# Optimization experiments

Measured on AMD Instinct MI355X. Metric: run time of the kernel, lower is better.

Reference implementation:

```python
import jax, jax.numpy as jnp
import numpy as np
import math

EPS = 1e-5
GROUPS = 32

def group_norm(x, gamma, beta, groups=GROUPS, eps=EPS):
    B, C, H, W = x.shape
    xr = x.reshape(B, groups, C // groups, H, W)
    m = xr.mean(axis=(2, 3, 4), keepdims=True)
    v = xr.var(axis=(2, 3, 4), keepdims=True)
    xr = (xr - m) * jax.lax.rsqrt(v + eps)
    x = xr.reshape(B, C, H, W)
    return x * gamma[None, :, None, None] + beta[None, :, None, None]

def swish(x):
    return x * jax.nn.sigmoid(x)

def conv2d(x, w, b=None, padding='SAME'):
    # x: NCHW, w: OIHW
    y = jax.lax.conv_general_dilated(x, w, window_strides=(1, 1), padding=padding,
                                     dimension_numbers=('NCHW', 'OIHW', 'NCHW'))
    if b is not None:
        y = y + b[None, :, None, None]
    return y

def setup_inputs() -> dict:
    key = jax.random.key(0)
    ks = jax.random.split(key, 24)
    B, C, H, W = 16, 256, 32, 32
    NE = 256  # noise_level_emb_dim
    s = 0.02
    inp = {
        'x': jax.random.normal(ks[0], (B, C, H, W), jnp.float32),
        'time_emb': jax.random.normal(ks[1], (B, NE), jnp.float32),
        'c': jax.random.normal(ks[2], (B, C, H, W), jnp.float32),
        # block1: GroupNorm + Swish + Conv3x3(dim -> dim_out)
        'gn1_g': jnp.ones((C,), jnp.float32),
        'gn1_b': jnp.zeros((C,), jnp.float32),
        'conv1_w': jax.random.normal(ks[3], (C, C, 3, 3), jnp.float32) * s,
        'conv1_b': jnp.zeros((C,), jnp.float32),
        # FeatureWiseAffine linear (use_affine_level=False): Linear(NE -> dim_out)
        'noise_w': jax.random.normal(ks[4], (C, NE), jnp.float32) * s,
        'noise_b': jnp.zeros((C,), jnp.float32),
        # block2: GroupNorm + Swish + Conv3x3(dim_out -> dim_out)
        'gn2_g': jnp.ones((C,), jnp.float32),
        'gn2_b': jnp.zeros((C,), jnp.float32),
        'conv2_w': jax.random.normal(ks[5], (C, C, 3, 3), jnp.float32) * s,
        'conv2_b': jnp.zeros((C,), jnp.float32),
        # c_func: Conv1x1(dim_out -> dim_out)
        'cfunc_w': jax.random.normal(ks[6], (C, C, 1, 1), jnp.float32) * s,
        'cfunc_b': jnp.zeros((C,), jnp.float32),
        # attention: GroupNorm, qkv Conv1x1 (no bias), out Conv1x1
        'attn_gn_g': jnp.ones((C,), jnp.float32),
        'attn_gn_b': jnp.zeros((C,), jnp.float32),
        'qkv_w': jax.random.normal(ks[7], (3 * C, C, 1, 1), jnp.float32) * s,
        'out_w': jax.random.normal(ks[8], (C, C, 1, 1), jnp.float32) * s,
        'out_b': jnp.zeros((C,), jnp.float32),
    }
    return inp

def reference(x, time_emb, c,
              gn1_g, gn1_b, conv1_w, conv1_b,
              noise_w, noise_b,
              gn2_g, gn2_b, conv2_w, conv2_b,
              cfunc_w, cfunc_b,
              attn_gn_g, attn_gn_b, qkv_w, out_w, out_b):
    B, C, H, W = x.shape
    # ---- ResnetBlock ----
    h = conv2d(swish(group_norm(x, gn1_g, gn1_b)), conv1_w, conv1_b)
    # FeatureWiseAffine (additive): h + Linear(time_emb) broadcast over HxW
    h = h + (time_emb @ noise_w.T + noise_b)[:, :, None, None]
    h = conv2d(swish(group_norm(h, gn2_g, gn2_b)), conv2_w, conv2_b)
    h = conv2d(c, cfunc_w, cfunc_b) + h
    h = h + x  # res_conv is Identity since dim == dim_out
    # ---- SelfAttention (n_head=1) ----
    n = group_norm(h, attn_gn_g, attn_gn_b)
    qkv = conv2d(n, qkv_w)                       # [B, 3C, H, W]
    q, k, v = jnp.split(qkv.reshape(B, 3 * C, H * W), 3, axis=1)  # each [B, C, HW]
    scores = jnp.einsum('bcs,bct->bst', q, k) / math.sqrt(C)      # [B, HW, HW]
    attn = jax.nn.softmax(scores, axis=-1)
    o = jnp.einsum('bst,bct->bcs', attn, v).reshape(B, C, H, W)
    o = conv2d(o, out_w, out_b)
    return o + h
```

## Files before the change

kernel.cpp:

```cpp
#include <hip/hip_runtime.h>
#include <hip/hip_bf16.h>
#include <math.h>

typedef __hip_bfloat16 bf16;
typedef short short8 __attribute__((ext_vector_type(8)));
typedef float floatx4 __attribute__((ext_vector_type(4)));

#define NB 16
#define NC 256
#define NHW 1024
#define NNE 256
#define NP (NB*NC*NHW)

__device__ __forceinline__ unsigned short f2bu(float f){
  bf16 h = (bf16)f; return *(unsigned short*)&h;
}

template<bool SWISH>
__global__ void gn_t_kernel(const float* __restrict__ src, const float* __restrict__ gamma,
                            const float* __restrict__ beta, short* __restrict__ xp){
  int b = blockIdx.x >> 5, g = blockIdx.x & 31;
  const int GSZ = 8*NHW;
  size_t base = ((size_t)b*NC + g*8)*NHW;
  int tid = threadIdx.x;
  float s = 0.f, ss = 0.f;
  for (int i = tid; i < GSZ; i += 256){
    float v = src[base+i];
    s += v; ss += v*v;
  }
  __shared__ float rs[256], rq[256];
  rs[tid] = s; rq[tid] = ss;
  __syncthreads();
  for (int off=128; off>0; off>>=1){
    if (tid < off){ rs[tid]+=rs[tid+off]; rq[tid]+=rq[tid+off]; }
    __syncthreads();
  }
  float mean = rs[0] * (1.f/GSZ);
  float var  = rq[0] * (1.f/GSZ) - mean*mean;
  float inv  = rsqrtf(var + 1e-5f);
  float gm[8], bt[8];
  #pragma unroll
  for (int j=0;j<8;j++){ gm[j] = gamma[g*8+j]*inv; bt[j] = beta[g*8+j]; }
  short* dst = xp + (((size_t)b*8 + (g>>2))*NHW)*32 + (g&3)*8;
  for (int px = tid; px < NHW; px += 256){
    short8 pk;
    #pragma unroll
    for (int j=0;j<8;j++){
      float v = (src[base + j*NHW + px] - mean)*gm[j] + bt[j];
      if (SWISH) v = v / (1.f + __expf(-v));
      pk[j] = (short)f2bu(v);
    }
    *(short8*)(dst + (size_t)px*32) = pk;
  }
}

template<bool SWISH>
__global__ void gn_post_kernel(const float* __restrict__ src, const float* __restrict__ st,
                               const float* __restrict__ gamma, const float* __restrict__ beta,
                               short* __restrict__ xp){
  int b = blockIdx.x >> 5, g = blockIdx.x & 31;
  size_t base = ((size_t)b*NC + g*8)*NHW;
  int tid = threadIdx.x;
  float s  = st[(b*32+g)*2+0];
  float ss = st[(b*32+g)*2+1];
  float mean = s * (1.f/8192.f);
  float var  = ss * (1.f/8192.f) - mean*mean;
  float inv  = rsqrtf(var + 1e-5f);
  float gm[8], bt[8];
  #pragma unroll
  for (int j=0;j<8;j++){ gm[j] = gamma[g*8+j]*inv; bt[j] = beta[g*8+j]; }
  short* dst = xp + (((size_t)b*8 + (g>>2))*NHW)*32 + (g&3)*8;
  for (int px = tid; px < NHW; px += 256){
    short8 pk;
    #pragma unroll
    for (int j=0;j<8;j++){
      float v = (src[base + j*NHW + px] - mean)*gm[j] + bt[j];
      if (SWISH) v = v / (1.f + __expf(-v));
      pk[j] = (short)f2bu(v);
    }
    *(short8*)(dst + (size_t)px*32) = pk;
  }
}

__global__ void wprep3_kernel(const float* __restrict__ w1, const float* __restrict__ w2,
                              short* __restrict__ wp1, short* __restrict__ wp2,
                              float* __restrict__ st){
  int co = blockIdx.x & 255;
  const float* w = (blockIdx.x < 256) ? w1 : w2;
  short* wp = (blockIdx.x < 256) ? wp1 : wp2;
  int tid = threadIdx.x;
  if (blockIdx.x == 0){
    for (int i=tid;i<2048;i+=256) st[i] = 0.f;
  }
  __shared__ float tmp[2304];
  for (int i=tid;i<2304;i+=256) tmp[i] = w[(size_t)co*2304 + i];
  __syncthreads();
  for (int j=tid;j<2304;j+=256){
    int tap = j>>8, ci = j&255;
    wp[(((size_t)tap*8 + (ci>>5))*NC + co)*32 + (ci&31)] = (short)f2bu(tmp[ci*9 + tap]);
  }
}

__global__ void wprep1_kernel(const float* __restrict__ wq, const float* __restrict__ wc,
                              const float* __restrict__ wo,
                              short* __restrict__ wqp, short* __restrict__ wcp,
                              short* __restrict__ wop){
  int blk = blockIdx.x, tid = threadIdx.x;
  if (blk < 768){
    float v = wq[(size_t)blk*256 + tid];
    wqp[(((size_t)(tid>>5))*768 + blk)*32 + (tid&31)] = (short)f2bu(v);
  } else if (blk < 1024){
    int co = blk - 768;
    float v = wc[(size_t)co*256 + tid];
    wcp[(((size_t)(tid>>5))*256 + co)*32 + (tid&31)] = (short)f2bu(v);
  } else {
    int co = blk - 1024;
    float v = wo[(size_t)co*256 + tid];
    wop[(((size_t)(tid>>5))*256 + co)*32 + (tid&31)] = (short)f2bu(v);
  }
}

__global__ void cvtc_kernel(const float* __restrict__ c_in, short* __restrict__ cp){
  int pxc = blockIdx.x, cc = blockIdx.y, b = blockIdx.z, tid = threadIdx.x;
  __shared__ float ld[32][257];
  size_t gbase = ((size_t)b*NC + cc*32)*NHW + pxc*256;
  for (int j=0;j<32;j++) ld[j][tid] = c_in[gbase + (size_t)j*NHW + tid];
  __syncthreads();
  short* dst = cp + (((size_t)b*8 + cc)*NHW + pxc*256)*32;
  for (int it=0;it<4;it++){
    int pxl = it*64 + (tid>>2), ckl = tid&3;
    short8 pk;
    #pragma unroll
    for (int e=0;e<8;e++) pk[e] = (short)f2bu(ld[ckl*8+e][pxl]);
    *(short8*)(dst + (size_t)pxl*32 + ckl*8) = pk;
  }
}

__global__ void noise_kernel(const float* __restrict__ emb, const float* __restrict__ w,
                             const float* __restrict__ bias, float* __restrict__ na){
  int b = blockIdx.x, c = threadIdx.x;
  __shared__ float e[NNE];
  e[c] = emb[b*NNE + c];
  __syncthreads();
  float acc = bias[c];
  for (int k=0;k<NNE;k++) acc += e[k]*w[c*NNE+k];
  na[b*NC + c] = acc;
}

#define XSTR 264
__global__ __launch_bounds__(256,2)
void conv3_mfma_kernel(const short* __restrict__ xp, const short* __restrict__ wp,
                       const float* __restrict__ bias, const float* __restrict__ bias_bc,
                       const float* __restrict__ addf, float* __restrict__ out,
                       float* __restrict__ st){
  const int b = blockIdx.y, y0 = blockIdx.x;
  const int tid = threadIdx.x, wave = tid>>6, lane = tid&63;
  const int quad = lane>>4, lm = lane&15;
  __shared__ short Xs[3*34*XSTR];

  if (tid < 192){
    int r = tid>>6, side = (tid>>5)&1, ck = tid&31;
    short8 z = {0,0,0,0,0,0,0,0};
    *(short8*)&Xs[((r*34) + side*33)*XSTR + ck*8] = z;
  }
  for (int it=0; it<12; ++it){
    int idx = it*256 + tid;
    int r = idx>>10, rem = idx&1023;
    int x = rem>>5, ch = rem&31;
    int y = y0 - 1 + r;
    short8 v = {0,0,0,0,0,0,0,0};
    if ((unsigned)y < 32u)
      v = *(const short8*)(xp + (((size_t)b*8 + (ch>>2))*NHW + y*32 + x)*32 + (ch&3)*8);
    *(short8*)&Xs[(r*34 + x + 1)*XSTR + ch*8] = v;
  }
  __syncthreads();

  floatx4 acc[4][2];
  #pragma unroll
  for (int mt=0;mt<4;mt++)
    #pragma unroll
    for (int nt=0;nt<2;nt++) acc[mt][nt] = (floatx4){0.f,0.f,0.f,0.f};

  const int co_w = wave*64;
  const int aoff = (co_w + lm)*32 + quad*8;

  auto ldA = [&](int j, short8 a[4]){
    const short* p = wp + (size_t)j*NC*32 + aoff;
    #pragma unroll
    for (int mt=0;mt<4;mt++) a[mt] = *(const short8*)(p + mt*(16*32));
  };
  auto ldB = [&](int j, short8 bf[2]){
    int tap = j>>3, kk = j&7;
    int dy = (tap*11)>>5;
    int dxp = tap - dy*3;
    int base = (lm+dxp)*XSTR + quad*8 + kk*32 + dy*(34*XSTR);
    #pragma unroll
    for (int nt=0;nt<2;nt++)
      bf[nt] = *(const short8*)&Xs[base + nt*(16*XSTR)];
  };

  short8 A[4][4], Bf[4][2];
  ldA(0,A[0]); ldB(0,Bf[0]);
  ldA(1,A[1]); ldB(1,Bf[1]);
  ldA(2,A[2]); ldB(2,Bf[2]);
  ldA(3,A[3]); ldB(3,Bf[3]);
  for (int it=0; it<72; it+=4){
    #pragma unroll
    for (int u=0;u<4;u++){
      #pragma unroll
      for (int mt=0;mt<4;mt++)
        #pragma unroll
        for (int nt=0;nt<2;nt++)
          acc[mt][nt] = __builtin_amdgcn_mfma_f32_16x16x32_bf16(A[u][mt], Bf[u][nt], acc[mt][nt], 0,0,0);
      int j = it + 4 + u; if (j > 71) j = 71;
      ldA(j, A[u]); ldB(j, Bf[u]);
    }
  }

  const int hw0 = y0*32;
  float gs[4], gq[4];
  #pragma unroll
  for (int mt=0;mt<4;mt++){ gs[mt]=0.f; gq[mt]=0.f; }
  #pragma unroll
  for (int mt=0;mt<4;mt++){
    #pragma unroll
    for (int r=0;r<4;r++){
      int co = co_w + mt*16 + quad*4 + r;
      float bb = bias[co] + (bias_bc ? bias_bc[b*NC + co] : 0.f);
      size_t ob = ((size_t)b*NC + co)*NHW + hw0;
      #pragma unroll
      for (int nt=0;nt<2;nt++){
        size_t oi = ob + nt*16 + lm;
        float v = acc[mt][nt][r] + bb;
        if (addf) v += addf[oi];
        out[oi] = v;
        gs[mt] += v; gq[mt] += v*v;
      }
    }
  }
  #pragma unroll
  for (int mt=0;mt<4;mt++){
    float s = gs[mt], q = gq[mt];
    #pragma unroll
    for (int o=1;o<32;o<<=1){ s += __shfl_xor(s, o, 64); q += __shfl_xor(q, o, 64); }
    if ((lane&31) == 0){
      int g = (co_w>>3) + mt*2 + (quad>>1);
      atomicAdd(&st[(b*32+g)*2+0], s);
      atomicAdd(&st[(b*32+g)*2+1], q);
    }
  }
}

__global__ __launch_bounds__(256)
void gemm_cfunc_kernel(const short* __restrict__ cp, const short* __restrict__ wcp,
                       const float* __restrict__ bias, const float* __restrict__ xres,
                       float* __restrict__ out){
  const int b = blockIdx.z;
  const int tid = threadIdx.x, wave = tid>>6, lane = tid&63;
  const int quad = lane>>4, lm = lane&15;
  const int M0 = blockIdx.y*128 + (wave>>1)*64;
  const int N0 = blockIdx.x*128 + (wave&1)*64;
  floatx4 acc[4][4];
  #pragma unroll
  for (int mt=0;mt<4;mt++)
    #pragma unroll
    for (int nt=0;nt<4;nt++) acc[mt][nt] = (floatx4){0.f,0.f,0.f,0.f};
  #pragma unroll
  for (int kk=0;kk<8;kk++){
    short8 af[4], bfr[4];
    #pragma unroll
    for (int mt=0;mt<4;mt++)
      af[mt] = *(const short8*)(wcp + ((size_t)kk*256 + M0 + mt*16 + lm)*32 + quad*8);
    #pragma unroll
    for (int nt=0;nt<4;nt++)
      bfr[nt] = *(const short8*)(cp + (((size_t)b*8 + kk)*NHW + N0 + nt*16 + lm)*32 + quad*8);
    #pragma unroll
    for (int mt=0;mt<4;mt++)
      #pragma unroll
      for (int nt=0;nt<4;nt++)
        acc[mt][nt] = __builtin_amdgcn_mfma_f32_16x16x32_bf16(af[mt], bfr[nt], acc[mt][nt], 0,0,0);
  }
  #pragma unroll
  for (int mt=0;mt<4;mt++){
    #pragma unroll
    for (int r=0;r<4;r++){
      int co = M0 + mt*16 + quad*4 + r;
      float bb = bias[co];
      size_t ob = ((size_t)b*NC + co)*NHW + N0;
      #pragma unroll
      for (int nt=0;nt<4;nt++){
        size_t oi = ob + nt*16 + lm;
        out[oi] = acc[mt][nt][r] + bb + xres[oi];
      }
    }
  }
}

__global__ __launch_bounds__(256)
void gemm_qkv_kernel(const short* __restrict__ ntp, const short* __restrict__ wqp,
                     short* __restrict__ qp, short* __restrict__ kp, short* __restrict__ vp){
  const int b = blockIdx.z;
  const int tid = threadIdx.x, wave = tid>>6, lane = tid&63;
  const int quad = lane>>4, lm = lane&15;
  const int M0 = blockIdx.y*128 + (wave>>1)*64;
  const int N0 = blockIdx.x*128 + (wave&1)*64;
  floatx4 acc[4][4];
  #pragma unroll
  for (int mt=0;mt<4;mt++)
    #pragma unroll
    for (int nt=0;nt<4;nt++) acc[mt][nt] = (floatx4){0.f,0.f,0.f,0.f};
  #pragma unroll
  for (int kk=0;kk<8;kk++){
    short8 af[4], bfr[4];
    #pragma unroll
    for (int mt=0;mt<4;mt++)
      af[mt] = *(const short8*)(wqp + ((size_t)kk*768 + M0 + mt*16 + lm)*32 + quad*8);
    #pragma unroll
    for (int nt=0;nt<4;nt++)
      bfr[nt] = *(const short8*)(ntp + (((size_t)b*8 + kk)*NHW + N0 + nt*16 + lm)*32 + quad*8);
    #pragma unroll
    for (int mt=0;mt<4;mt++)
      #pragma unroll
      for (int nt=0;nt<4;nt++)
        acc[mt][nt] = __builtin_amdgcn_mfma_f32_16x16x32_bf16(af[mt], bfr[nt], acc[mt][nt], 0,0,0);
  }
  #pragma unroll
  for (int mt=0;mt<4;mt++){
    int co_base = M0 + mt*16 + quad*4;
    int sec = co_base >> 8;
    int c = co_base & 255;
    #pragma unroll
    for (int nt=0;nt<4;nt++){
      int s = N0 + nt*16 + lm;
      if (sec < 2){
        unsigned short t0 = f2bu(acc[mt][nt][0]), t1 = f2bu(acc[mt][nt][1]);
        unsigned short t2 = f2bu(acc[mt][nt][2]), t3 = f2bu(acc[mt][nt][3]);
        uint2 w2; w2.x = ((unsigned)t1<<16)|t0; w2.y = ((unsigned)t3<<16)|t2;
        short* dst = (sec==0) ? qp : kp;
        *(uint2*)(dst + (((size_t)b*8 + (c>>5))*NHW + s)*32 + (c&31)) = w2;
      } else {
        #pragma unroll
        for (int r=0;r<4;r++)
          vp[(((size_t)b*32 + (s>>5))*NC + c + r)*32 + (s&31)] = (short)f2bu(acc[mt][nt][r]);
      }
    }
  }
}

__global__ __launch_bounds__(1024)
void attn_mfma_kernel(const short* __restrict__ qp, const short* __restrict__ kp,
                      const short* __restrict__ vp, short* __restrict__ op){
  const int bx = blockIdx.x;
  const int b = bx & 15;
  const int s0 = (bx >> 4) * 64;
  const int tid = threadIdx.x, wave = tid>>6, lane = tid&63;
  const int quad = lane>>4, lm = lane&15;

  __shared__ short P[64*1024];
  __shared__ float red[64][16];
  __shared__ float fred[64];

  floatx4 sc[4][4];
  #pragma unroll
  for (int rt=0;rt<4;rt++)
    #pragma unroll
    for (int ti=0;ti<4;ti++) sc[rt][ti] = (floatx4){0.f,0.f,0.f,0.f};

  const int colb = wave*64;
  #pragma unroll
  for (int h=0;h<8;h++){
    const size_t hb = ((size_t)b*8 + h)*NHW;
    short8 aq[4], kf[4];
    #pragma unroll
    for (int rt=0;rt<4;rt++)
      aq[rt] = *(const short8*)(qp + (hb + s0 + rt*16 + lm)*32 + quad*8);
    #pragma unroll
    for (int ti=0;ti<4;ti++)
      kf[ti] = *(const short8*)(kp + (hb + colb + ti*16 + lm)*32 + quad*8);
    #pragma unroll
    for (int rt=0;rt<4;rt++)
      #pragma unroll
      for (int ti=0;ti<4;ti++)
        sc[rt][ti] = __builtin_amdgcn_mfma_f32_16x16x32_bf16(aq[rt], kf[ti], sc[rt][ti], 0,0,0);
  }

  const float scale = 0.0625f;
  float mx[4][4];
  #pragma unroll
  for (int rt=0;rt<4;rt++)
    #pragma unroll
    for (int r=0;r<4;r++) mx[rt][r] = -1e30f;
  #pragma unroll
  for (int rt=0;rt<4;rt++)
    #pragma unroll
    for (int ti=0;ti<4;ti++)
      #pragma unroll
      for (int r=0;r<4;r++){
        float v = sc[rt][ti][r]*scale;
        sc[rt][ti][r] = v;
        mx[rt][r] = fmaxf(mx[rt][r], v);
      }
  #pragma unroll
  for (int o=1;o<16;o<<=1)
    #pragma unroll
    for (int rt=0;rt<4;rt++)
      #pragma unroll
      for (int r=0;r<4;r++) mx[rt][r] = fmaxf(mx[rt][r], __shfl_xor(mx[rt][r], o, 64));
  if (lm==0){
    #pragma unroll
    for (int rt=0;rt<4;rt++)
      #pragma unroll
      for (int r=0;r<4;r++) red[rt*16 + quad*4 + r][wave] = mx[rt][r];
  }
  __syncthreads();
  {
    float v = red[tid>>4][tid&15];
    #pragma unroll
    for (int o=1;o<16;o<<=1) v = fmaxf(v, __shfl_xor(v, o, 64));
    if ((tid&15)==0) fred[tid>>4] = v;
  }
  __syncthreads();
  float fmr[4][4], sm[4][4];
  #pragma unroll
  for (int rt=0;rt<4;rt++)
    #pragma unroll
    for (int r=0;r<4;r++){ fmr[rt][r] = fred[rt*16 + quad*4 + r]; sm[rt][r] = 0.f; }
  #pragma unroll
  for (int rt=0;rt<4;rt++)
    #pragma unroll
    for (int ti=0;ti<4;ti++)
      #pragma unroll
      for (int r=0;r<4;r++){
        float e = __expf(sc[rt][ti][r] - fmr[rt][r]);
        sc[rt][ti][r] = e;
        sm[rt][r] += e;
      }
  #pragma unroll
  for (int o=1;o<16;o<<=1)
    #pragma unroll
    for (int rt=0;rt<4;rt++)
      #pragma unroll
      for (int r=0;r<4;r++) sm[rt][r] += __shfl_xor(sm[rt][r], o, 64);
  __syncthreads();
  if (lm==0){
    #pragma unroll
    for (int rt=0;rt<4;rt++)
      #pragma unroll
      for (int r=0;r<4;r++) red[rt*16 + quad*4 + r][wave] = sm[rt][r];
  }
  __syncthreads();
  {
    float v = red[tid>>4][tid&15];
    #pragma unroll
    for (int o=1;o<16;o<<=1) v += __shfl_xor(v, o, 64);
    if ((tid&15)==0) fred[tid>>4] = 1.f/v;
  }
  __syncthreads();
  float fir[4][4];
  #pragma unroll
  for (int rt=0;rt<4;rt++)
    #pragma unroll
    for (int r=0;r<4;r++) fir[rt][r] = fred[rt*16 + quad*4 + r];
  #pragma unroll
  for (int rt=0;rt<4;rt++)
    #pragma unroll
    for (int ti=0;ti<4;ti++)
      #pragma unroll
      for (int r=0;r<4;r++){
        int row = rt*16 + quad*4 + r;
        int col = colb + ti*16 + lm;
        int off = row*1024 + ((((col>>3) ^ (row&7))&127)<<3) + (col&7);
        P[off] = (short)f2bu(sc[rt][ti][r]*fir[rt][r]);
      }
  __syncthreads();

  const int cg = wave>>1, sh = wave&1;
  const int ch0 = cg*32;
  floatx4 oacc[2][2];
  #pragma unroll
  for (int mt=0;mt<2;mt++)
    #pragma unroll
    for (int nt=0;nt<2;nt++) oacc[mt][nt] = (floatx4){0.f,0.f,0.f,0.f};

  #pragma unroll
  for (int kk=0;kk<32;kk++){
    short8 pf[2], vf[2];
    #pragma unroll
    for (int mt=0;mt<2;mt++){
      int row = sh*32 + mt*16 + lm;
      int off = row*1024 + ((((kk*4 + quad) ^ (row&7))&127)<<3);
      pf[mt] = *(const short8*)(&P[off]);
    }
    #pragma unroll
    for (int nt=0;nt<2;nt++)
      vf[nt] = *(const short8*)(vp + (((size_t)b*32 + kk)*NC + ch0 + nt*16 + lm)*32 + quad*8);
    #pragma unroll
    for (int mt=0;mt<2;mt++)
      #pragma unroll
      for (int nt=0;nt<2;nt++)
        oacc[mt][nt] = __builtin_amdgcn_mfma_f32_16x16x32_bf16(pf[mt], vf[nt], oacc[mt][nt], 0,0,0);
  }

  #pragma unroll
  for (int nt=0;nt<2;nt++){
    int c = ch0 + nt*16 + lm;
    int cc = c>>5, cl = c&31;
    #pragma unroll
    for (int mt=0;mt<2;mt++)
      #pragma unroll
      for (int r=0;r<4;r++){
        int s = s0 + sh*32 + mt*16 + quad*4 + r;
        op[(((size_t)b*8 + cc)*NHW + s)*32 + cl] = (short)f2bu(oacc[mt][nt][r]);
      }
  }
}

__global__ __launch_bounds__(256)
void outproj_mfma_kernel(const short* __restrict__ op, const short* __restrict__ wop,
                         const float* __restrict__ obias, const float* __restrict__ h,
                         float* __restrict__ out){
  const int b = blockIdx.z;
  const int tid = threadIdx.x, wave = tid>>6, lane = tid&63;
  const int quad = lane>>4, lm = lane&15;
  const int M0 = blockIdx.y*128 + (wave>>1)*64;
  const int N0 = blockIdx.x*128 + (wave&1)*64;
  floatx4 acc[4][4];
  #pragma unroll
  for (int mt=0;mt<4;mt++)
    #pragma unroll
    for (int nt=0;nt<4;nt++) acc[mt][nt] = (floatx4){0.f,0.f,0.f,0.f};
  #pragma unroll
  for (int kk=0;kk<8;kk++){
    short8 af[4], bfr[4];
    #pragma unroll
    for (int mt=0;mt<4;mt++)
      af[mt] = *(const short8*)(wop + ((size_t)kk*256 + M0 + mt*16 + lm)*32 + quad*8);
    #pragma unroll
    for (int nt=0;nt<4;nt++)
      bfr[nt] = *(const short8*)(op + (((size_t)b*8 + kk)*NHW + N0 + nt*16 + lm)*32 + quad*8);
    #pragma unroll
    for (int mt=0;mt<4;mt++)
      #pragma unroll
      for (int nt=0;nt<4;nt++)
        acc[mt][nt] = __builtin_amdgcn_mfma_f32_16x16x32_bf16(af[mt], bfr[nt], acc[mt][nt], 0,0,0);
  }
  #pragma unroll
  for (int mt=0;mt<4;mt++){
    #pragma unroll
    for (int r=0;r<4;r++){
      int co = M0 + mt*16 + quad*4 + r;
      float bb = obias[co];
      size_t ob = ((size_t)b*NC + co)*NHW + N0;
      #pragma unroll
      for (int nt=0;nt<4;nt++){
        size_t oi = ob + nt*16 + lm;
        out[oi] = acc[mt][nt][r] + bb + h[oi];
      }
    }
  }
}

extern "C" void kernel_launch(void* const* d_in, const int* in_sizes, int n_in,
                              void* d_out, int out_size, void* d_ws, size_t ws_size,
                              hipStream_t stream){
  const float* x        = (const float*)d_in[0];
  const float* time_emb = (const float*)d_in[1];
  const float* c_in     = (const float*)d_in[2];
  const float* gn1_g    = (const float*)d_in[3];
  const float* gn1_b    = (const float*)d_in[4];
  const float* conv1_w  = (const float*)d_in[5];
  const float* conv1_b  = (const float*)d_in[6];
  const float* noise_w  = (const float*)d_in[7];
  const float* noise_b  = (const float*)d_in[8];
  const float* gn2_g    = (const float*)d_in[9];
  const float* gn2_b    = (const float*)d_in[10];
  const float* conv2_w  = (const float*)d_in[11];
  const float* conv2_b  = (const float*)d_in[12];
  const float* cfunc_w  = (const float*)d_in[13];
  const float* cfunc_b  = (const float*)d_in[14];
  const float* agn_g    = (const float*)d_in[15];
  const float* agn_b    = (const float*)d_in[16];
  const float* qkv_w    = (const float*)d_in[17];
  const float* out_w    = (const float*)d_in[18];
  const float* out_b    = (const float*)d_in[19];
  float* outp = (float*)d_out;

  float* ws = (float*)d_ws;
  float* buf_h = ws;
  float* buf_t = buf_h + NP;
  short* xpb   = (short*)(buf_t + NP);
  short* qp    = xpb + NP;
  short* kp    = qp + NP;
  short* vp    = kp + NP;
  short* wp1   = vp + NP;
  short* wp2   = wp1 + 589824;
  short* wqp   = wp2 + 589824;
  short* wcp   = wqp + 196608;
  short* wop   = wcp + 65536;
  float* na    = (float*)(wop + 65536);
  float* st    = na + NB*NC;
  float* st2   = st;
  float* st3   = st + 1024;
  short* cp    = (short*)buf_t;
  short* op    = (short*)buf_t;

  wprep3_kernel<<<512, 256, 0, stream>>>(conv1_w, conv2_w, wp1, wp2, st);
  wprep1_kernel<<<1280, 256, 0, stream>>>(qkv_w, cfunc_w, out_w, wqp, wcp, wop);
  cvtc_kernel<<<dim3(4,8,NB), 256, 0, stream>>>(c_in, cp);
  noise_kernel<<<NB, 256, 0, stream>>>(time_emb, noise_w, noise_b, na);
  gn_t_kernel<true><<<NB*32, 256, 0, stream>>>(x, gn1_g, gn1_b, xpb);
  conv3_mfma_kernel<<<dim3(32, NB), 256, 0, stream>>>(xpb, wp1, conv1_b, na, nullptr, buf_h, st2);
  gn_post_kernel<true><<<NB*32, 256, 0, stream>>>(buf_h, st2, gn2_g, gn2_b, xpb);
  gemm_cfunc_kernel<<<dim3(8,2,NB), 256, 0, stream>>>(cp, wcp, cfunc_b, x, buf_h);
  conv3_mfma_kernel<<<dim3(32, NB), 256, 0, stream>>>(xpb, wp2, conv2_b, nullptr, buf_h, buf_h, st3);
  gn_post_kernel<false><<<NB*32, 256, 0, stream>>>(buf_h, st3, agn_g, agn_b, xpb);
  gemm_qkv_kernel<<<dim3(8,6,NB), 256, 0, stream>>>(xpb, wqp, qp, kp, vp);
  attn_mfma_kernel<<<256, 1024, 0, stream>>>(qp, kp, vp, op);
  outproj_mfma_kernel<<<dim3(8,2,NB), 256, 0, stream>>>(op, wop, out_b, buf_h, outp);
}
```

Baseline: 375.7 us.

## Drop LDS staging in 3x3 conv and read activations directly from global

The 3x3 conv kernel no longer stages a haloed three-row input tile in shared memory. Each wave now loads its B fragments straight from global memory, masking out-of-bounds taps with zeros. The grid is retiled so each block covers 128 output channels by 64 pixels instead of 256 channels by one row. This removes the LDS fill, the barrier and the software-pipelined fragment prefetch, but relies on cache hits for the ninefold tap reuse and loses the explicit prefetch that hid load latency.

Result: slower. 398.0 us (+5.9%).

```diff
diff --git a/kernel.cpp b/kernel.cpp
--- a/kernel.cpp
+++ b/kernel.cpp
@@ -147,33 +147,17 @@
   na[b*NC + c] = acc;
 }
 
-#define XSTR 264
 __global__ __launch_bounds__(256,2)
 void conv3_mfma_kernel(const short* __restrict__ xp, const short* __restrict__ wp,
                        const float* __restrict__ bias, const float* __restrict__ bias_bc,
                        const float* __restrict__ addf, float* __restrict__ out,
                        float* __restrict__ st){
-  const int b = blockIdx.y, y0 = blockIdx.x;
+  const int b = blockIdx.z, bx = blockIdx.x, by = blockIdx.y;
   const int tid = threadIdx.x, wave = tid>>6, lane = tid&63;
   const int quad = lane>>4, lm = lane&15;
-  __shared__ short Xs[3*34*XSTR];
-
-  if (tid < 192){
-    int r = tid>>6, side = (tid>>5)&1, ck = tid&31;
-    short8 z = {0,0,0,0,0,0,0,0};
-    *(short8*)&Xs[((r*34) + side*33)*XSTR + ck*8] = z;
-  }
-  for (int it=0; it<12; ++it){
-    int idx = it*256 + tid;
-    int r = idx>>10, rem = idx&1023;
-    int x = rem>>5, ch = rem&31;
-    int y = y0 - 1 + r;
-    short8 v = {0,0,0,0,0,0,0,0};
-    if ((unsigned)y < 32u)
-      v = *(const short8*)(xp + (((size_t)b*8 + (ch>>2))*NHW + y*32 + x)*32 + (ch&3)*8);
-    *(short8*)&Xs[(r*34 + x + 1)*XSTR + ch*8] = v;
-  }
-  __syncthreads();
+  const int co_w = by*128 + (wave>>1)*64;
+  const int hw0  = bx*64 + (wave&1)*32;
+  const int py   = bx*2 + (wave&1);
 
   floatx4 acc[4][2];
   #pragma unroll
@@ -181,43 +165,44 @@
     #pragma unroll
     for (int nt=0;nt<2;nt++) acc[mt][nt] = (floatx4){0.f,0.f,0.f,0.f};
 
-  const int co_w = wave*64;
-  const int aoff = (co_w + lm)*32 + quad*8;
-
-  auto ldA = [&](int j, short8 a[4]){
-    const short* p = wp + (size_t)j*NC*32 + aoff;
-    #pragma unroll
-    for (int mt=0;mt<4;mt++) a[mt] = *(const short8*)(p + mt*(16*32));
-  };
-  auto ldB = [&](int j, short8 bf[2]){
-    int tap = j>>3, kk = j&7;
-    int dy = (tap*11)>>5;
-    int dxp = tap - dy*3;
-    int base = (lm+dxp)*XSTR + quad*8 + kk*32 + dy*(34*XSTR);
-    #pragma unroll
-    for (int nt=0;nt<2;nt++)
-      bf[nt] = *(const short8*)&Xs[base + nt*(16*XSTR)];
-  };
-
-  short8 A[4][4], Bf[4][2];
-  ldA(0,A[0]); ldB(0,Bf[0]);
-  ldA(1,A[1]); ldB(1,Bf[1]);
-  ldA(2,A[2]); ldB(2,Bf[2]);
-  ldA(3,A[3]); ldB(3,Bf[3]);
-  for (int it=0; it<72; it+=4){
-    #pragma unroll
-    for (int u=0;u<4;u++){
+  const short8 z8 = {0,0,0,0,0,0,0,0};
+  const short* wbase = wp + ((size_t)(co_w + lm))*32 + quad*8;
+  const short* xbb   = xp + ((size_t)b*8)*NHW*32;
+
+  #pragma unroll
+  for (int tap=0; tap<9; tap++){
+    const int dy = tap/3 - 1, dx = tap%3 - 1;
+    const int sy = py + dy;
+    const bool yok = ((unsigned)sy < 32u);
+    bool ok[2];
+    int off[2];
+    #pragma unroll
+    for (int nt=0;nt<2;nt++){
+      int xc = nt*16 + lm + dx;
+      ok[nt]  = yok && ((unsigned)xc < 32u);
+      off[nt] = ok[nt] ? ((sy*32 + xc)*32 + quad*8) : 0;
+    }
+    #pragma unroll
+    for (int cc=0; cc<8; cc++){
+      const short* wb = wbase + ((size_t)(tap*8+cc))*NC*32;
+      short8 af[4];
+      #pragma unroll
+      for (int mt=0;mt<4;mt++) af[mt] = *(const short8*)(wb + mt*(16*32));
+      const short* xb = xbb + (size_t)cc*NHW*32;
+      short8 bfr[2];
+      #pragma unroll
+      for (int nt=0;nt<2;nt++){
+        short8 v = *(const short8*)(xb + off[nt]);
+        bfr[nt] = ok[nt] ? v : z8;
+      }
       #pragma unroll
       for (int mt=0;mt<4;mt++)
         #pragma unroll
         for (int nt=0;nt<2;nt++)
-          acc[mt][nt] = __builtin_amdgcn_mfma_f32_16x16x32_bf16(A[u][mt], Bf[u][nt], acc[mt][nt], 0,0,0);
-      int j = it + 4 + u; if (j > 71) j = 71;
-      ldA(j, A[u]); ldB(j, Bf[u]);
-    }
-  }
-
-  const int hw0 = y0*32;
+          acc[mt][nt] = __builtin_amdgcn_mfma_f32_16x16x32_bf16(af[mt], bfr[nt], acc[mt][nt], 0,0,0);
+    }
+  }
+
   float gs[4], gq[4];
   #pragma unroll
   for (int mt=0;mt<4;mt++){ gs[mt]=0.f; gq[mt]=0.f; }
@@ -609,10 +594,10 @@
   cvtc_kernel<<<dim3(4,8,NB), 256, 0, stream>>>(c_in, cp);
   noise_kernel<<<NB, 256, 0, stream>>>(time_emb, noise_w, noise_b, na);
   gn_t_kernel<true><<<NB*32, 256, 0, stream>>>(x, gn1_g, gn1_b, xpb);
-  conv3_mfma_kernel<<<dim3(32, NB), 256, 0, stream>>>(xpb, wp1, conv1_b, na, nullptr, buf_h, st2);
+  conv3_mfma_kernel<<<dim3(16, 2, NB), 256, 0, stream>>>(xpb, wp1, conv1_b, na, nullptr, buf_h, st2);
   gn_post_kernel<true><<<NB*32, 256, 0, stream>>>(buf_h, st2, gn2_g, gn2_b, xpb);
   gemm_cfunc_kernel<<<dim3(8,2,NB), 256, 0, stream>>>(cp, wcp, cfunc_b, x, buf_h);
-  conv3_mfma_kernel<<<dim3(32, NB), 256, 0, stream>>>(xpb, wp2, conv2_b, nullptr, buf_h, buf_h, st3);
+  conv3_mfma_kernel<<<dim3(16, 2, NB), 256, 0, stream>>>(xpb, wp2, conv2_b, nullptr, buf_h, buf_h, st3);
   gn_post_kernel<false><<<NB*32, 256, 0, stream>>>(buf_h, st3, agn_g, agn_b, xpb);
   gemm_qkv_kernel<<<dim3(8,6,NB), 256, 0, stream>>>(xpb, wqp, qp, kp, vp);
   attn_mfma_kernel<<<256, 1024, 0, stream>>>(qp, kp, vp, op);
```
